# Optimization experiments

Measured on AMD Instinct MI355X. Metric: run time of the kernel, lower is better.

The kernel has to match this reference:

```python
import jax, jax.numpy as jnp
import numpy as np

B, S, T = 4, 1024, 1024
HID, ATT, NH = 1024, 1024, 16
HD = ATT // NH  # head size 64


def setup_inputs() -> dict:
    key = jax.random.key(0)
    ks = jax.random.split(key, 12)
    sc = 1.0 / np.sqrt(HID)
    return {
        "src": jax.random.normal(ks[0], (B, S, HID), jnp.float32),
        "tgt": jax.random.normal(ks[1], (B, T, HID), jnp.float32),
        "src_mask": jax.random.randint(ks[2], (B, S), 0, 2) > 0,
        "tgt_mask": jax.random.randint(ks[3], (B, T), 0, 2) > 0,
        "qw": jax.random.normal(ks[4], (ATT, HID), jnp.float32) * sc,
        "qb": jnp.zeros((ATT,), jnp.float32),
        "kw": jax.random.normal(ks[5], (ATT, HID), jnp.float32) * sc,
        "kb": jnp.zeros((ATT,), jnp.float32),
        "vw": jax.random.normal(ks[6], (ATT, HID), jnp.float32) * sc,
        "vb": jnp.zeros((ATT,), jnp.float32),
        "ow": jax.random.normal(ks[7], (HID, ATT), jnp.float32) * (1.0 / np.sqrt(ATT)),
        "ob": jnp.zeros((HID,), jnp.float32),
    }


def _heads(x, w, b, L):
    # x:[B,L,HID] -> [B,NH,L,HD]
    return (x @ w.T + b).reshape(B, L, NH, HD).transpose(0, 2, 1, 3)


def reference(src, tgt, src_mask, tgt_mask, qw, qb, kw, kb, vw, vb, ow, ob):
    q = _heads(src, qw, qb, S)
    k = _heads(tgt, kw, kb, T)
    v_src = _heads(src, vw, vb, S)
    v_tgt = _heads(tgt, vw, vb, T)

    attn = jnp.einsum("bhsd,bhtd->bhst", q, k) / np.sqrt(HD)  # shared scores

    sm = src_mask[:, None, :, None].astype(attn.dtype)  # [B,1,S,1]
    tm = tgt_mask[:, None, None, :].astype(attn.dtype)  # [B,1,1,T]
    NEG = 100000.0
    attn_src = attn * sm - NEG * (1.0 - sm)
    attn_tgt = attn * tm - NEG * (1.0 - tm)

    p_src = jax.nn.softmax(attn_src, axis=-1)                        # [B,H,S,T]
    p_tgt = jax.nn.softmax(attn_tgt.swapaxes(-1, -2), axis=-1)       # [B,H,T,S]

    o_src = jnp.einsum("bhst,bhtd->bhsd", p_src, v_tgt)
    o_tgt = jnp.einsum("bhts,bhsd->bhtd", p_tgt, v_src)

    o_src = o_src.transpose(0, 2, 1, 3).reshape(B, S, ATT) @ ow.T + ob
    o_tgt = o_tgt.transpose(0, 2, 1, 3).reshape(B, T, ATT) @ ow.T + ob
    return (o_src, o_tgt)
```

## Files before the change

### kernel.cpp

```cpp
#include <hip/hip_runtime.h>
#include <stdint.h>

typedef _Float16 f16;
typedef _Float16 f16x8 __attribute__((ext_vector_type(8)));
typedef _Float16 f16x4 __attribute__((ext_vector_type(4)));
typedef __fp16   h16x2 __attribute__((ext_vector_type(2)));
typedef float    f32x4 __attribute__((ext_vector_type(4)));

#define MFMA_F16(A, B, C) __builtin_amdgcn_mfma_f32_16x16x32_f16((A), (B), (C), 0, 0, 0)

__device__ __forceinline__ void gload_lds16(const void* g, void* l) {
  __builtin_amdgcn_global_load_lds((const __attribute__((address_space(1))) void*)g,
                                   (__attribute__((address_space(3))) void*)l, 16, 0, 0);
}

__global__ void cvt_f32_f16(const float* __restrict__ s0, const float* __restrict__ s1,
                            const float* __restrict__ s2, const float* __restrict__ s3,
                            const float* __restrict__ s4, const float* __restrict__ s5,
                            f16* __restrict__ d0, f16* __restrict__ d1, f16* __restrict__ d2,
                            f16* __restrict__ d3, f16* __restrict__ d4, f16* __restrict__ d5) {
  const float* sp; f16* dp; int n4;
  switch (blockIdx.y) {
    case 0:  sp = s0; dp = d0; n4 = (4096 * 1024) / 4; break;
    case 1:  sp = s1; dp = d1; n4 = (4096 * 1024) / 4; break;
    case 2:  sp = s2; dp = d2; n4 = (1024 * 1024) / 4; break;
    case 3:  sp = s3; dp = d3; n4 = (1024 * 1024) / 4; break;
    case 4:  sp = s4; dp = d4; n4 = (1024 * 1024) / 4; break;
    default: sp = s5; dp = d5; n4 = (1024 * 1024) / 4; break;
  }
  int stride = gridDim.x * blockDim.x;
  for (int i = blockIdx.x * blockDim.x + threadIdx.x; i < n4; i += stride) {
    f32x4 v = *(const f32x4*)(sp + (size_t)i * 4);
    f16x4 h;
    h[0] = (f16)v[0]; h[1] = (f16)v[1]; h[2] = (f16)v[2]; h[3] = (f16)v[3];
    *(f16x4*)(dp + (size_t)i * 4) = h;
  }
}

__device__ __forceinline__ void gemm_core_k1024(const f16* __restrict__ A, const f16* __restrict__ W,
                                                f16* lA, f16* lB, f32x4 (&acc)[4][4],
                                                int row0, int col0) {
  const int tid = threadIdx.x;
  const int lane = tid & 63;
  const int w = tid >> 6;
  const int g = lane >> 4, c = lane & 15;
  const int wr = (w >> 1) * 64, wc = (w & 1) * 64;

  int sr[2], scol[2];
#pragma unroll
  for (int p = 0; p < 2; ++p) {
    int slot = p * 256 + tid;
    int r = slot >> 2, sph = slot & 3;
    sr[p] = r;
    scol[p] = (sph ^ ((r >> 1) & 3)) * 8;
  }
  const f16* Abase = A + (size_t)row0 * 1024;
  const f16* Wbase = W + (size_t)col0 * 1024;

  auto STAGE = [&](int nb, int k0) {
#pragma unroll
    for (int p = 0; p < 2; ++p) {
      gload_lds16(Abase + (size_t)sr[p] * 1024 + k0 + scol[p],
                  lA + nb * (128 * 32) + (p * 256 + w * 64) * 8);
      gload_lds16(Wbase + (size_t)sr[p] * 1024 + k0 + scol[p],
                  lB + nb * (128 * 32) + (p * 256 + w * 64) * 8);
    }
  };

  STAGE(0, 0);
  STAGE(1, 32);

  int cur = 0;
  for (int kt = 0; kt < 32; ++kt) {
    if (kt < 31) {
      asm volatile("s_waitcnt vmcnt(4)" ::: "memory");
    } else {
      asm volatile("s_waitcnt vmcnt(0)" ::: "memory");
    }
    __builtin_amdgcn_s_barrier();
    __builtin_amdgcn_sched_barrier(0);
    if (kt < 30) {
      int nxt2 = (cur >= 1) ? cur - 1 : 2;
      STAGE(nxt2, (kt + 2) * 32);
    }

    const f16* cA = lA + cur * (128 * 32);
    const f16* cB = lB + cur * (128 * 32);
    f16x8 af[4], bf[4];
#pragma unroll
    for (int m = 0; m < 4; ++m) {
      int r = wr + m * 16 + c;
      af[m] = *(const f16x8*)(cA + r * 32 + (g ^ ((r >> 1) & 3)) * 8);
    }
#pragma unroll
    for (int n = 0; n < 4; ++n) {
      int r = wc + n * 16 + c;
      bf[n] = *(const f16x8*)(cB + r * 32 + (g ^ ((r >> 1) & 3)) * 8);
    }
    __builtin_amdgcn_s_setprio(1);
#pragma unroll
    for (int m = 0; m < 4; ++m)
#pragma unroll
      for (int n = 0; n < 4; ++n)
        acc[m][n] = MFMA_F16(af[m], bf[n], acc[m][n]);
    __builtin_amdgcn_s_setprio(0);

    cur = (cur < 2) ? cur + 1 : 0;
  }
}

__global__ __launch_bounds__(256, 2) void proj_gemm(
    const f16* __restrict__ src16, const f16* __restrict__ tgt16,
    const f16* __restrict__ qw16, const f16* __restrict__ kw16, const f16* __restrict__ vw16,
    const float* __restrict__ qb, const float* __restrict__ kb, const float* __restrict__ vb,
    f16* __restrict__ q16, f16* __restrict__ k16, f16* __restrict__ vtS, f16* __restrict__ vtT) {
  __shared__ f16 lA[2 * 128 * 32];
  __shared__ f16 lB1[2 * 128 * 32];
  __shared__ f16 lB2[2 * 128 * 32];
  const int lin = blockIdx.x;
  const int xcd = lin & 7;
  const int slot = lin >> 3;
  const int pr = xcd >> 2;
  const int y = (xcd & 3) * 8 + (slot >> 3);
  const int x = slot & 7;

  const f16* A  = pr ? tgt16 : src16;
  const f16* W1 = pr ? kw16 : qw16;
  const float* b1 = pr ? kb : qb;
  f16* O1 = pr ? k16 : q16;
  f16* O2 = pr ? vtT : vtS;
  const int row0 = y * 128;
  const int col0 = x * 128;

  const int tid = threadIdx.x;
  const int lane = tid & 63;
  const int w = tid >> 6;
  const int g = lane >> 4, c = lane & 15;
  const int wr = (w >> 1) * 64, wc = (w & 1) * 64;

  int sr[2], scol[2];
#pragma unroll
  for (int p = 0; p < 2; ++p) {
    int slt = p * 256 + tid;
    int r = slt >> 2, sph = slt & 3;
    sr[p] = r;
    scol[p] = (sph ^ ((r >> 1) & 3)) * 8;
  }
  const f16* Abase  = A + (size_t)row0 * 1024;
  const f16* W1base = W1 + (size_t)col0 * 1024;
  const f16* W2base = vw16 + (size_t)col0 * 1024;

  auto STAGE = [&](int nb, int k0) {
#pragma unroll
    for (int p = 0; p < 2; ++p) {
      gload_lds16(Abase + (size_t)sr[p] * 1024 + k0 + scol[p],
                  lA + nb * (128 * 32) + (p * 256 + w * 64) * 8);
      gload_lds16(W1base + (size_t)sr[p] * 1024 + k0 + scol[p],
                  lB1 + nb * (128 * 32) + (p * 256 + w * 64) * 8);
      gload_lds16(W2base + (size_t)sr[p] * 1024 + k0 + scol[p],
                  lB2 + nb * (128 * 32) + (p * 256 + w * 64) * 8);
    }
  };

  f32x4 acc1[4][4] = {};
  f32x4 acc2[4][4] = {};

  STAGE(0, 0);

  for (int kt = 0; kt < 32; ++kt) {
    const int cur = kt & 1;
    asm volatile("s_waitcnt vmcnt(0)" ::: "memory");
    __builtin_amdgcn_s_barrier();
    __builtin_amdgcn_sched_barrier(0);
    if (kt < 31) STAGE(cur ^ 1, (kt + 1) * 32);

    const f16* cA = lA + cur * (128 * 32);
    const f16* cB1 = lB1 + cur * (128 * 32);
    const f16* cB2 = lB2 + cur * (128 * 32);
    f16x8 af[4], bf1[4], bf2[4];
#pragma unroll
    for (int m = 0; m < 4; ++m) {
      int r = wr + m * 16 + c;
      af[m] = *(const f16x8*)(cA + r * 32 + (g ^ ((r >> 1) & 3)) * 8);
    }
#pragma unroll
    for (int n = 0; n < 4; ++n) {
      int r = wc + n * 16 + c;
      int off = r * 32 + (g ^ ((r >> 1) & 3)) * 8;
      bf1[n] = *(const f16x8*)(cB1 + off);
      bf2[n] = *(const f16x8*)(cB2 + off);
    }
    __builtin_amdgcn_s_setprio(1);
#pragma unroll
    for (int m = 0; m < 4; ++m)
#pragma unroll
      for (int n = 0; n < 4; ++n) {
        acc1[m][n] = MFMA_F16(af[m], bf1[n], acc1[m][n]);
        acc2[m][n] = MFMA_F16(af[m], bf2[n], acc2[m][n]);
      }
    __builtin_amdgcn_s_setprio(0);
  }

#pragma unroll
  for (int n = 0; n < 4; ++n) {
    int colg = col0 + wc + n * 16 + c;
    float bv = b1[colg];
#pragma unroll
    for (int m = 0; m < 4; ++m) {
      int rb = row0 + wr + m * 16 + g * 4;
#pragma unroll
      for (int r = 0; r < 4; ++r)
        O1[(size_t)(rb + r) * 1024 + colg] = (f16)(acc1[m][n][r] + bv);
    }
  }
#pragma unroll
  for (int n = 0; n < 4; ++n) {
    int colg = col0 + wc + n * 16 + c;
    float bv = vb[colg];
#pragma unroll
    for (int m = 0; m < 4; ++m) {
      int row = row0 + wr + m * 16 + g * 4;
      int bb = row >> 10, t = row & 1023;
      int tl = t & 63;
      int tp = (t & ~63) + (tl & 32) + ((tl & 12) << 1) + ((tl & 16) >> 2) + (tl & 3);
      f16x4 pk;
#pragma unroll
      for (int r = 0; r < 4; ++r) pk[r] = (f16)(acc2[m][n][r] + bv);
      *(f16x4*)(O2 + ((size_t)(bb << 10) + colg) * 1024 + tp) = pk;
    }
  }
}

__global__ __launch_bounds__(256, 2) void out_gemm(
    const f16* __restrict__ opre, const f16* __restrict__ ow16,
    const float* __restrict__ ob, float* __restrict__ out) {
  __shared__ f16 lA[3 * 128 * 32];
  __shared__ f16 lB[3 * 128 * 32];
  const int lin = blockIdx.x;
  const int xcd = lin & 7;
  const int slot = lin >> 3;
  const int y = xcd * 8 + (slot >> 3);
  const int x = slot & 7;
  const int row0 = y * 128;
  const int col0 = x * 128;
  f32x4 acc[4][4] = {};
  gemm_core_k1024(opre, ow16, lA, lB, acc, row0, col0);
  const int lane = threadIdx.x & 63;
  const int w = threadIdx.x >> 6;
  const int g = lane >> 4, c = lane & 15;
  const int wr = (w >> 1) * 64, wc = (w & 1) * 64;
#pragma unroll
  for (int n = 0; n < 4; ++n) {
    int colg = col0 + wc + n * 16 + c;
    float bv = ob[colg];
#pragma unroll
    for (int m = 0; m < 4; ++m) {
      int rb = row0 + wr + m * 16 + g * 4;
#pragma unroll
      for (int r = 0; r < 4; ++r)
        out[(size_t)(rb + r) * 1024 + colg] = acc[m][n][r] + bv;
    }
  }
}

__global__ __launch_bounds__(256, 2) void attn_fwd(
    const f16* __restrict__ q16, const f16* __restrict__ k16,
    const f16* __restrict__ vtS, const f16* __restrict__ vtT,
    const int* __restrict__ smask, const int* __restrict__ tmask,
    f16* __restrict__ opre) {
  const int bid = blockIdx.x;
  const int xcd = bid & 7;
  const int idx = bid >> 3;
  const int bhp = xcd * 16 + (idx >> 2);
  const int qblk = idx & 3;
  const int pass = bhp >> 6;
  const int bh = bhp & 63;
  const int b = bh >> 4, h = bh & 15;

  const f16* Q  = pass ? k16 : q16;
  const f16* Kt = pass ? q16 : k16;
  const f16* VT = pass ? vtS : vtT;
  const int* qmask = pass ? tmask : smask;
  const int outRowOff = pass ? 4096 : 0;

  const int tid = threadIdx.x;
  const int lane = tid & 63, wv = tid >> 6;
  const int g = lane >> 4, c = lane & 15;
  const int qrow0 = qblk * 256 + wv * 64;

  __shared__ f16 lK[2][64 * 64];
  __shared__ f16 lV[2][64 * 64];

  const size_t kbase = (size_t)b * (1024 * 1024) + h * 64;
  const size_t vbase = (size_t)bh * (64 * 1024);

  const float SC2 = 0.18033688f;
  f16x8 qf[4][2];
#pragma unroll
  for (int m = 0; m < 4; ++m) {
    f16 sh = (f16)(qmask[b * 1024 + qrow0 + m * 16 + c] ? SC2 : 0.0f);
#pragma unroll
    for (int kc = 0; kc < 2; ++kc) {
      f16x8 v = *(const f16x8*)(Q + ((size_t)(b * 1024 + qrow0 + m * 16 + c)) * 1024 + h * 64 + kc * 32 + g * 8);
#pragma unroll
      for (int j = 0; j < 8; ++j) v[j] *= sh;
      qf[m][kc] = v;
    }
  }

  auto STAGE = [&](int nb, int t0) {
#pragma unroll
    for (int i = 0; i < 2; ++i) {
      int p = i * 256 + tid;
      int row = p >> 3;
      int u = (p & 7) ^ (row & 7);
      gload_lds16(Kt + kbase + (size_t)(t0 + row) * 1024 + u * 8, &lK[nb][(i * 256 + wv * 64) * 8]);
      gload_lds16(VT + vbase + (size_t)row * 1024 + t0 + u * 8, &lV[nb][(i * 256 + wv * 64) * 8]);
    }
  };

  f32x4 accO[4][4] = {};
  float lpart[4] = {0.0f, 0.0f, 0.0f, 0.0f};

  STAGE(0, 0);

  for (int tt = 0; tt < 16; ++tt) {
    asm volatile("s_waitcnt vmcnt(0)" ::: "memory");
    __builtin_amdgcn_s_barrier();
    __builtin_amdgcn_sched_barrier(0);
    if (tt < 15) STAGE((tt + 1) & 1, (tt + 1) * 64);
    const f16* curK = lK[tt & 1];
    const f16* curV = lV[tt & 1];

    f16x8 kf[4][2];
#pragma unroll
    for (int n = 0; n < 4; ++n) {
      int row = n * 16 + c;
#pragma unroll
      for (int kc = 0; kc < 2; ++kc)
        kf[n][kc] = *(const f16x8*)(curK + row * 64 + (((kc * 4 + g) ^ (row & 7)) * 8));
    }

    f16x8 vf[4][2];
#pragma unroll
    for (int nd = 0; nd < 4; ++nd) {
      int row = nd * 16 + c;
#pragma unroll
      for (int kc = 0; kc < 2; ++kc)
        vf[nd][kc] = *(const f16x8*)(curV + row * 64 + (((kc * 4 + g) ^ (row & 7)) * 8));
    }

    f16x8 pa[4][2];
#pragma unroll
    for (int m = 0; m < 4; ++m) {
      f32x4 sc[4];
      __builtin_amdgcn_s_setprio(1);
#pragma unroll
      for (int n = 0; n < 4; ++n) {
        f32x4 z = {0.0f, 0.0f, 0.0f, 0.0f};
        z = MFMA_F16(kf[n][0], qf[m][0], z);
        sc[n] = MFMA_F16(kf[n][1], qf[m][1], z);
      }
      __builtin_amdgcn_s_setprio(0);
      float e[16];
#pragma unroll
      for (int n = 0; n < 4; ++n)
#pragma unroll
        for (int r = 0; r < 4; ++r) e[n * 4 + r] = __builtin_amdgcn_exp2f(sc[n][r]);
      float s8[8];
#pragma unroll
      for (int i = 0; i < 8; ++i) s8[i] = e[i] + e[i + 8];
      float s4[4];
#pragma unroll
      for (int i = 0; i < 4; ++i) s4[i] = s8[i] + s8[i + 4];
      lpart[m] += (s4[0] + s4[1]) + (s4[2] + s4[3]);
      union PU { f16x8 v; h16x2 h[4]; } u0, u1;
#pragma unroll
      for (int i = 0; i < 4; ++i) {
        u0.h[i] = __builtin_amdgcn_cvt_pkrtz(e[2 * i], e[2 * i + 1]);
        u1.h[i] = __builtin_amdgcn_cvt_pkrtz(e[8 + 2 * i], e[9 + 2 * i]);
      }
      pa[m][0] = u0.v;
      pa[m][1] = u1.v;
    }

    __builtin_amdgcn_s_setprio(1);
#pragma unroll
    for (int m = 0; m < 4; ++m)
#pragma unroll
      for (int nd = 0; nd < 4; ++nd) {
        accO[m][nd] = MFMA_F16(pa[m][0], vf[nd][0], accO[m][nd]);
        accO[m][nd] = MFMA_F16(pa[m][1], vf[nd][1], accO[m][nd]);
      }
    __builtin_amdgcn_s_setprio(0);
  }

#pragma unroll
  for (int m = 0; m < 4; ++m) {
    float ls = lpart[m];
    ls += __shfl_xor(ls, 16);
    ls += __shfl_xor(ls, 32);
#pragma unroll
    for (int r = 0; r < 4; ++r) {
      float lr = __shfl(ls, 20 * g + r);
      float inv = 1.0f / lr;
      size_t orow = (size_t)(outRowOff + b * 1024 + qrow0 + m * 16 + 4 * g + r);
#pragma unroll
      for (int nd = 0; nd < 4; ++nd)
        opre[orow * 1024 + h * 64 + nd * 16 + c] = (f16)(accO[m][nd][r] * inv);
    }
  }
}

extern "C" void kernel_launch(void* const* d_in, const int* in_sizes, int n_in,
                              void* d_out, int out_size, void* d_ws, size_t ws_size,
                              hipStream_t stream) {
  (void)in_sizes; (void)n_in; (void)out_size; (void)ws_size;
  const float* src = (const float*)d_in[0];
  const float* tgt = (const float*)d_in[1];
  const int*   smask = (const int*)d_in[2];
  const int*   tmask = (const int*)d_in[3];
  const float* qw = (const float*)d_in[4];
  const float* qb = (const float*)d_in[5];
  const float* kw = (const float*)d_in[6];
  const float* kb = (const float*)d_in[7];
  const float* vw = (const float*)d_in[8];
  const float* vb = (const float*)d_in[9];
  const float* ow = (const float*)d_in[10];
  const float* ob = (const float*)d_in[11];
  float* out = (float*)d_out;

  f16* wsp = (f16*)d_ws;
  const size_t M4 = (size_t)4096 * 1024;
  const size_t M1 = (size_t)1024 * 1024;
  f16* src16 = wsp;
  f16* tgt16 = src16 + M4;
  f16* qw16  = tgt16 + M4;
  f16* kw16  = qw16 + M1;
  f16* vw16  = kw16 + M1;
  f16* ow16  = vw16 + M1;
  f16* q16   = ow16 + M1;
  f16* k16   = q16 + M4;
  f16* vtS   = k16 + M4;
  f16* vtT   = vtS + M4;
  f16* opre  = wsp;

  cvt_f32_f16<<<dim3(512, 6), 256, 0, stream>>>(src, tgt, qw, kw, vw, ow,
                                                src16, tgt16, qw16, kw16, vw16, ow16);
  proj_gemm<<<dim3(512), 256, 0, stream>>>(src16, tgt16, qw16, kw16, vw16,
                                           qb, kb, vb, q16, k16, vtS, vtT);
  attn_fwd<<<dim3(512), 256, 0, stream>>>(q16, k16, vtS, vtT, smask, tmask, opre);
  out_gemm<<<dim3(512), 256, 0, stream>>>(opre, ow16, ob, out);
}
```

Measured before the change: 121.7 us.

## Fuse activation fp32->fp16 conversion into projection GEMM and widen attention KV tiles

The projection GEMM now reads src/tgt directly in fp32 through registers, converts them to fp16, and writes them to LDS. The separate conversion pass and its fp16 activation round trip are gone, so the conversion kernel only handles the weights. The attention kernel stages 128 keys/values per iteration instead of 64, halving the number of barrier/stage rounds at the cost of doubling LDS per buffer. The register-path A load adds register pressure and replaces async global-to-LDS loads with a synchronous write plus an lgkmcnt wait.

```diff
diff --git a/kernel.cpp b/kernel.cpp
--- a/kernel.cpp
+++ b/kernel.cpp
@@ -16,18 +16,16 @@
 
 __global__ void cvt_f32_f16(const float* __restrict__ s0, const float* __restrict__ s1,
                             const float* __restrict__ s2, const float* __restrict__ s3,
-                            const float* __restrict__ s4, const float* __restrict__ s5,
-                            f16* __restrict__ d0, f16* __restrict__ d1, f16* __restrict__ d2,
-                            f16* __restrict__ d3, f16* __restrict__ d4, f16* __restrict__ d5) {
-  const float* sp; f16* dp; int n4;
+                            f16* __restrict__ d0, f16* __restrict__ d1,
+                            f16* __restrict__ d2, f16* __restrict__ d3) {
+  const float* sp; f16* dp;
   switch (blockIdx.y) {
-    case 0:  sp = s0; dp = d0; n4 = (4096 * 1024) / 4; break;
-    case 1:  sp = s1; dp = d1; n4 = (4096 * 1024) / 4; break;
-    case 2:  sp = s2; dp = d2; n4 = (1024 * 1024) / 4; break;
-    case 3:  sp = s3; dp = d3; n4 = (1024 * 1024) / 4; break;
-    case 4:  sp = s4; dp = d4; n4 = (1024 * 1024) / 4; break;
-    default: sp = s5; dp = d5; n4 = (1024 * 1024) / 4; break;
-  }
+    case 0:  sp = s0; dp = d0; break;
+    case 1:  sp = s1; dp = d1; break;
+    case 2:  sp = s2; dp = d2; break;
+    default: sp = s3; dp = d3; break;
+  }
+  const int n4 = (1024 * 1024) / 4;
   int stride = gridDim.x * blockDim.x;
   for (int i = blockIdx.x * blockDim.x + threadIdx.x; i < n4; i += stride) {
     f32x4 v = *(const f32x4*)(sp + (size_t)i * 4);
@@ -110,7 +108,7 @@
 }
 
 __global__ __launch_bounds__(256, 2) void proj_gemm(
-    const f16* __restrict__ src16, const f16* __restrict__ tgt16,
+    const float* __restrict__ srcF, const float* __restrict__ tgtF,
     const f16* __restrict__ qw16, const f16* __restrict__ kw16, const f16* __restrict__ vw16,
     const float* __restrict__ qb, const float* __restrict__ kb, const float* __restrict__ vb,
     f16* __restrict__ q16, f16* __restrict__ k16, f16* __restrict__ vtS, f16* __restrict__ vtT) {
@@ -124,7 +122,7 @@
   const int y = (xcd & 3) * 8 + (slot >> 3);
   const int x = slot & 7;
 
-  const f16* A  = pr ? tgt16 : src16;
+  const float* A = pr ? tgtF : srcF;
   const f16* W1 = pr ? kw16 : qw16;
   const float* b1 = pr ? kb : qb;
   f16* O1 = pr ? k16 : q16;
@@ -146,15 +144,34 @@
     sr[p] = r;
     scol[p] = (sph ^ ((r >> 1) & 3)) * 8;
   }
-  const f16* Abase  = A + (size_t)row0 * 1024;
+  const float* Abase = A + (size_t)row0 * 1024;
   const f16* W1base = W1 + (size_t)col0 * 1024;
   const f16* W2base = vw16 + (size_t)col0 * 1024;
 
-  auto STAGE = [&](int nb, int k0) {
+  f32x4 areg[2][2];
+
+  auto LOADA = [&](int k0) {
 #pragma unroll
     for (int p = 0; p < 2; ++p) {
-      gload_lds16(Abase + (size_t)sr[p] * 1024 + k0 + scol[p],
-                  lA + nb * (128 * 32) + (p * 256 + w * 64) * 8);
+      const float* ap = Abase + (size_t)sr[p] * 1024 + k0 + scol[p];
+      areg[p][0] = *(const f32x4*)ap;
+      areg[p][1] = *(const f32x4*)(ap + 4);
+    }
+  };
+  auto WRITEA = [&](int nb) {
+#pragma unroll
+    for (int p = 0; p < 2; ++p) {
+      union { f16x8 v; h16x2 h[4]; } u;
+      u.h[0] = __builtin_amdgcn_cvt_pkrtz(areg[p][0][0], areg[p][0][1]);
+      u.h[1] = __builtin_amdgcn_cvt_pkrtz(areg[p][0][2], areg[p][0][3]);
+      u.h[2] = __builtin_amdgcn_cvt_pkrtz(areg[p][1][0], areg[p][1][1]);
+      u.h[3] = __builtin_amdgcn_cvt_pkrtz(areg[p][1][2], areg[p][1][3]);
+      *(f16x8*)(lA + nb * (128 * 32) + (p * 256 + tid) * 8) = u.v;
+    }
+  };
+  auto STAGEB = [&](int nb, int k0) {
+#pragma unroll
+    for (int p = 0; p < 2; ++p) {
       gload_lds16(W1base + (size_t)sr[p] * 1024 + k0 + scol[p],
                   lB1 + nb * (128 * 32) + (p * 256 + w * 64) * 8);
       gload_lds16(W2base + (size_t)sr[p] * 1024 + k0 + scol[p],
@@ -165,14 +182,18 @@
   f32x4 acc1[4][4] = {};
   f32x4 acc2[4][4] = {};
 
-  STAGE(0, 0);
+  LOADA(0);
+  STAGEB(0, 0);
 
   for (int kt = 0; kt < 32; ++kt) {
     const int cur = kt & 1;
     asm volatile("s_waitcnt vmcnt(0)" ::: "memory");
+    WRITEA(cur);
+    if (kt < 31) LOADA((kt + 1) * 32);
+    asm volatile("s_waitcnt lgkmcnt(0)" ::: "memory");
     __builtin_amdgcn_s_barrier();
     __builtin_amdgcn_sched_barrier(0);
-    if (kt < 31) STAGE(cur ^ 1, (kt + 1) * 32);
+    if (kt < 31) STAGEB(cur ^ 1, (kt + 1) * 32);
 
     const f16* cA = lA + cur * (128 * 32);
     const f16* cB1 = lB1 + cur * (128 * 32);
@@ -288,8 +309,8 @@
   const int g = lane >> 4, c = lane & 15;
   const int qrow0 = qblk * 256 + wv * 64;
 
-  __shared__ f16 lK[2][64 * 64];
-  __shared__ f16 lV[2][64 * 64];
+  __shared__ f16 lK[2][128 * 64];
+  __shared__ f16 lV[2][64 * 128];
 
   const size_t kbase = (size_t)b * (1024 * 1024) + h * 64;
   const size_t vbase = (size_t)bh * (64 * 1024);
@@ -310,12 +331,14 @@
 
   auto STAGE = [&](int nb, int t0) {
 #pragma unroll
-    for (int i = 0; i < 2; ++i) {
+    for (int i = 0; i < 4; ++i) {
       int p = i * 256 + tid;
-      int row = p >> 3;
-      int u = (p & 7) ^ (row & 7);
-      gload_lds16(Kt + kbase + (size_t)(t0 + row) * 1024 + u * 8, &lK[nb][(i * 256 + wv * 64) * 8]);
-      gload_lds16(VT + vbase + (size_t)row * 1024 + t0 + u * 8, &lV[nb][(i * 256 + wv * 64) * 8]);
+      int rowK = p >> 3;
+      int uK = (p & 7) ^ (rowK & 7);
+      gload_lds16(Kt + kbase + (size_t)(t0 + rowK) * 1024 + uK * 8, &lK[nb][(i * 256 + wv * 64) * 8]);
+      int rowV = p >> 4;
+      int uV = (p & 15) ^ (rowV & 7);
+      gload_lds16(VT + vbase + (size_t)rowV * 1024 + t0 + uV * 8, &lV[nb][(i * 256 + wv * 64) * 8]);
     }
   };
 
@@ -324,75 +347,78 @@
 
   STAGE(0, 0);
 
-  for (int tt = 0; tt < 16; ++tt) {
+  for (int tt = 0; tt < 8; ++tt) {
     asm volatile("s_waitcnt vmcnt(0)" ::: "memory");
     __builtin_amdgcn_s_barrier();
     __builtin_amdgcn_sched_barrier(0);
-    if (tt < 15) STAGE((tt + 1) & 1, (tt + 1) * 64);
+    if (tt < 7) STAGE((tt + 1) & 1, (tt + 1) * 128);
     const f16* curK = lK[tt & 1];
     const f16* curV = lV[tt & 1];
 
-    f16x8 kf[4][2];
-#pragma unroll
-    for (int n = 0; n < 4; ++n) {
-      int row = n * 16 + c;
-#pragma unroll
-      for (int kc = 0; kc < 2; ++kc)
-        kf[n][kc] = *(const f16x8*)(curK + row * 64 + (((kc * 4 + g) ^ (row & 7)) * 8));
-    }
-
-    f16x8 vf[4][2];
-#pragma unroll
-    for (int nd = 0; nd < 4; ++nd) {
-      int row = nd * 16 + c;
-#pragma unroll
-      for (int kc = 0; kc < 2; ++kc)
-        vf[nd][kc] = *(const f16x8*)(curV + row * 64 + (((kc * 4 + g) ^ (row & 7)) * 8));
-    }
-
-    f16x8 pa[4][2];
-#pragma unroll
-    for (int m = 0; m < 4; ++m) {
-      f32x4 sc[4];
+#pragma unroll
+    for (int ts = 0; ts < 2; ++ts) {
+      f16x8 kf[4][2];
+#pragma unroll
+      for (int n = 0; n < 4; ++n) {
+        int row = ts * 64 + n * 16 + c;
+#pragma unroll
+        for (int kc = 0; kc < 2; ++kc)
+          kf[n][kc] = *(const f16x8*)(curK + row * 64 + (((kc * 4 + g) ^ (row & 7)) * 8));
+      }
+
+      f16x8 vf[4][2];
+#pragma unroll
+      for (int nd = 0; nd < 4; ++nd) {
+        int row = nd * 16 + c;
+#pragma unroll
+        for (int kc = 0; kc < 2; ++kc)
+          vf[nd][kc] = *(const f16x8*)(curV + row * 128 + ((ts * 8 + ((kc * 4 + g) ^ (row & 7))) * 8));
+      }
+
+      f16x8 pa[4][2];
+#pragma unroll
+      for (int m = 0; m < 4; ++m) {
+        f32x4 sc[4];
+        __builtin_amdgcn_s_setprio(1);
+#pragma unroll
+        for (int n = 0; n < 4; ++n) {
+          f32x4 z = {0.0f, 0.0f, 0.0f, 0.0f};
+          z = MFMA_F16(kf[n][0], qf[m][0], z);
+          sc[n] = MFMA_F16(kf[n][1], qf[m][1], z);
+        }
+        __builtin_amdgcn_s_setprio(0);
+        float e[16];
+#pragma unroll
+        for (int n = 0; n < 4; ++n)
+#pragma unroll
+          for (int r = 0; r < 4; ++r) e[n * 4 + r] = __builtin_amdgcn_exp2f(sc[n][r]);
+        float s8[8];
+#pragma unroll
+        for (int i = 0; i < 8; ++i) s8[i] = e[i] + e[i + 8];
+        float s4[4];
+#pragma unroll
+        for (int i = 0; i < 4; ++i) s4[i] = s8[i] + s8[i + 4];
+        lpart[m] += (s4[0] + s4[1]) + (s4[2] + s4[3]);
+        union PU { f16x8 v; h16x2 h[4]; } u0, u1;
+#pragma unroll
+        for (int i = 0; i < 4; ++i) {
+          u0.h[i] = __builtin_amdgcn_cvt_pkrtz(e[2 * i], e[2 * i + 1]);
+          u1.h[i] = __builtin_amdgcn_cvt_pkrtz(e[8 + 2 * i], e[9 + 2 * i]);
+        }
+        pa[m][0] = u0.v;
+        pa[m][1] = u1.v;
+      }
+
       __builtin_amdgcn_s_setprio(1);
 #pragma unroll
-      for (int n = 0; n < 4; ++n) {
-        f32x4 z = {0.0f, 0.0f, 0.0f, 0.0f};
-        z = MFMA_F16(kf[n][0], qf[m][0], z);
-        sc[n] = MFMA_F16(kf[n][1], qf[m][1], z);
-      }
+      for (int m = 0; m < 4; ++m)
+#pragma unroll
+        for (int nd = 0; nd < 4; ++nd) {
+          accO[m][nd] = MFMA_F16(pa[m][0], vf[nd][0], accO[m][nd]);
+          accO[m][nd] = MFMA_F16(pa[m][1], vf[nd][1], accO[m][nd]);
+        }
       __builtin_amdgcn_s_setprio(0);
-      float e[16];
-#pragma unroll
-      for (int n = 0; n < 4; ++n)
-#pragma unroll
-        for (int r = 0; r < 4; ++r) e[n * 4 + r] = __builtin_amdgcn_exp2f(sc[n][r]);
-      float s8[8];
-#pragma unroll
-      for (int i = 0; i < 8; ++i) s8[i] = e[i] + e[i + 8];
-      float s4[4];
-#pragma unroll
-      for (int i = 0; i < 4; ++i) s4[i] = s8[i] + s8[i + 4];
-      lpart[m] += (s4[0] + s4[1]) + (s4[2] + s4[3]);
-      union PU { f16x8 v; h16x2 h[4]; } u0, u1;
-#pragma unroll
-      for (int i = 0; i < 4; ++i) {
-        u0.h[i] = __builtin_amdgcn_cvt_pkrtz(e[2 * i], e[2 * i + 1]);
-        u1.h[i] = __builtin_amdgcn_cvt_pkrtz(e[8 + 2 * i], e[9 + 2 * i]);
-      }
-      pa[m][0] = u0.v;
-      pa[m][1] = u1.v;
-    }
-
-    __builtin_amdgcn_s_setprio(1);
-#pragma unroll
-    for (int m = 0; m < 4; ++m)
-#pragma unroll
-      for (int nd = 0; nd < 4; ++nd) {
-        accO[m][nd] = MFMA_F16(pa[m][0], vf[nd][0], accO[m][nd]);
-        accO[m][nd] = MFMA_F16(pa[m][1], vf[nd][1], accO[m][nd]);
-      }
-    __builtin_amdgcn_s_setprio(0);
+    }
   }
 
 #pragma unroll
@@ -433,9 +459,8 @@
   f16* wsp = (f16*)d_ws;
   const size_t M4 = (size_t)4096 * 1024;
   const size_t M1 = (size_t)1024 * 1024;
-  f16* src16 = wsp;
-  f16* tgt16 = src16 + M4;
-  f16* qw16  = tgt16 + M4;
+  f16* opre  = wsp;
+  f16* qw16  = wsp + 2 * M4;
   f16* kw16  = qw16 + M1;
   f16* vw16  = kw16 + M1;
   f16* ow16  = vw16 + M1;
@@ -443,11 +468,9 @@
   f16* k16   = q16 + M4;
   f16* vtS   = k16 + M4;
   f16* vtT   = vtS + M4;
-  f16* opre  = wsp;
-
-  cvt_f32_f16<<<dim3(512, 6), 256, 0, stream>>>(src, tgt, qw, kw, vw, ow,
-                                                src16, tgt16, qw16, kw16, vw16, ow16);
-  proj_gemm<<<dim3(512), 256, 0, stream>>>(src16, tgt16, qw16, kw16, vw16,
+
+  cvt_f32_f16<<<dim3(256, 4), 256, 0, stream>>>(qw, kw, vw, ow, qw16, kw16, vw16, ow16);
+  proj_gemm<<<dim3(512), 256, 0, stream>>>(src, tgt, qw16, kw16, vw16,
                                            qb, kb, vb, q16, k16, vtS, vtT);
   attn_fwd<<<dim3(512), 256, 0, stream>>>(q16, k16, vtS, vtT, smask, tmask, opre);
   out_gemm<<<dim3(512), 256, 0, stream>>>(opre, ow16, ob, out);
```

Measured after the change: 198.7 us. 63.2% more time.
